# Performance work log

Measured on AMD Instinct MI355X. Metric: run time of the kernel, lower is better.

## Reference

```python
import jax, jax.numpy as jnp
import numpy as np

B, LOOKBACK, N_STOCKS, D_MODEL, D_K, D_V, MAX_LAG = 64, 32, 256, 512, 128, 128, 16


def setup_inputs() -> dict:
    key = jax.random.key(0)
    ks = jax.random.split(key, 7)
    return {
        "query_stock_emb": jax.random.normal(ks[0], (B, D_MODEL), dtype=jnp.float32),
        "all_stock_embs": jax.random.normal(ks[1], (B, LOOKBACK, N_STOCKS, D_MODEL), dtype=jnp.float32),
        "W_q": jax.random.normal(ks[2], (D_K, D_MODEL), dtype=jnp.float32) * 0.02,
        "W_k": jax.random.normal(ks[3], (D_K, D_MODEL), dtype=jnp.float32) * 0.02,
        "W_v": jax.random.normal(ks[4], (D_V, D_MODEL), dtype=jnp.float32) * 0.02,
        "lags": jax.random.uniform(ks[5], (N_STOCKS,), dtype=jnp.float32) * MAX_LAG,
        "causal_gates": jax.random.normal(ks[6], (N_STOCKS,), dtype=jnp.float32) * 0.1,
        "max_lag": MAX_LAG,
    }


def reference(query_stock_emb, all_stock_embs, W_q, W_k, W_v, lags, causal_gates, max_lag):
    lookback = all_stock_embs.shape[1]
    n_stocks = all_stock_embs.shape[2]
    d_k = W_q.shape[0]

    q = query_stock_emb @ W_q.T                        # (B, d_k)
    gates = jax.nn.sigmoid(causal_gates)               # (S,)
    lag = jax.nn.sigmoid(lags) * max_lag               # (S,)

    lag_floor = jnp.clip(jnp.floor(lag), 0, lookback - 1).astype(jnp.int32)
    lag_ceil = jnp.clip(jnp.ceil(lag), 0, lookback - 1).astype(jnp.int32)
    alpha = lag - lag_floor.astype(lag.dtype)          # (S,)

    s_idx = jnp.arange(n_stocks)
    emb_floor = all_stock_embs[:, lag_floor, s_idx, :]  # (B, S, D)
    emb_ceil = all_stock_embs[:, lag_ceil, s_idx, :]    # (B, S, D)
    a = alpha[None, :, None]
    stock_emb = (1.0 - a) * emb_floor + a * emb_ceil    # (B, S, D)

    k = jnp.einsum("bsd,kd->bsk", stock_emb, W_k)       # (B, S, d_k)
    v = jnp.einsum("bsd,vd->bsv", stock_emb, W_v)       # (B, S, d_v)

    scores = jnp.einsum("bk,bsk->bs", q, k) / np.sqrt(d_k).astype(jnp.float32)
    scores = scores * gates[None, :]
    attn = jax.nn.softmax(scores, axis=1)               # (B, S)
    context = jnp.einsum("bs,bsv->bv", attn, v)         # (B, d_v)
    return context
```

## Files before the change

kernel.cpp:

```cpp
#include <hip/hip_runtime.h>
#include <math.h>

#define B_    64
#define LOOKB 32
#define NS    256
#define DM    512
#define DK    128
#define DV    128

__device__ __forceinline__ float sigmoidf_(float x) {
    return 1.0f / (1.0f + expf(-x));
}

__device__ __forceinline__ float load_maxlag(const void* p) {
    int vi = *(const int*)p;
    if (vi >= 0 && vi < (1 << 23)) return (float)vi;
    return *(const float*)p;
}

__device__ __forceinline__ void lag_params(const float* __restrict__ lags,
                                           float maxlag, int s,
                                           int& lf, int& lc, float& alpha) {
    float lag = sigmoidf_(lags[s]) * maxlag;
    float lf_f = fminf(fmaxf(floorf(lag), 0.0f), (float)(LOOKB - 1));
    float lc_f = fminf(fmaxf(ceilf(lag), 0.0f), (float)(LOOKB - 1));
    lf = (int)lf_f;
    lc = (int)lc_f;
    alpha = lag - lf_f;
}

__global__ void k_prep(const float* __restrict__ query,
                       const float* __restrict__ Wq,
                       const float* __restrict__ Wk,
                       float* __restrict__ ws_m) {
    __shared__ float qe[DM];
    __shared__ float qv[DK];
    const int b = blockIdx.x;
    const int tid = threadIdx.x;

    qe[tid]       = query[b * DM + tid];
    qe[tid + 256] = query[b * DM + tid + 256];
    __syncthreads();

    if (tid < DK) {
        const float4* wr = (const float4*)(Wq + (size_t)tid * DM);
        const float4* qr = (const float4*)qe;
        float acc = 0.f;
#pragma unroll 8
        for (int i = 0; i < DM / 4; ++i) {
            float4 w = wr[i], q4 = qr[i];
            acc += w.x * q4.x + w.y * q4.y + w.z * q4.z + w.w * q4.w;
        }
        qv[tid] = acc;
    }
    __syncthreads();

    for (int d = tid; d < DM; d += 256) {
        float acc = 0.f;
#pragma unroll 8
        for (int k = 0; k < DK; ++k)
            acc += qv[k] * Wk[(size_t)k * DM + d];
        ws_m[b * DM + d] = acc;
    }
}

__global__ void k_scores(const float* __restrict__ embs,
                         const float* __restrict__ lags,
                         const float* __restrict__ gates,
                         const void*  __restrict__ maxlag_p,
                         const float* __restrict__ ws_m,
                         float* __restrict__ ws_scores) {
    const int tid  = threadIdx.x;
    const int b     = blockIdx.x >> 6;
    const int sbase = (blockIdx.x & 63) << 2;
    const int wave  = tid >> 6;
    const int lane  = tid & 63;
    const int s     = sbase + wave;

    const float maxlag = load_maxlag(maxlag_p);
    int lf, lc; float alpha;
    lag_params(lags, maxlag, s, lf, lc, alpha);
    const float gate = sigmoidf_(gates[s]);

    const size_t off = (size_t)lane * 8;
    const float* mrow = ws_m + (size_t)b * DM + off;
    float4 m0 = *(const float4*)(mrow);
    float4 m1 = *(const float4*)(mrow + 4);

    const size_t bf = (((size_t)b * LOOKB + lf) * NS + s) * (size_t)DM + off;
    const size_t bc = (((size_t)b * LOOKB + lc) * NS + s) * (size_t)DM + off;
    float4 f0 = *(const float4*)(embs + bf);
    float4 f1 = *(const float4*)(embs + bf + 4);
    float4 c0 = *(const float4*)(embs + bc);
    float4 c1 = *(const float4*)(embs + bc + 4);

    float acc = m0.x * (f0.x + alpha * (c0.x - f0.x))
              + m0.y * (f0.y + alpha * (c0.y - f0.y))
              + m0.z * (f0.z + alpha * (c0.z - f0.z))
              + m0.w * (f0.w + alpha * (c0.w - f0.w))
              + m1.x * (f1.x + alpha * (c1.x - f1.x))
              + m1.y * (f1.y + alpha * (c1.y - f1.y))
              + m1.z * (f1.z + alpha * (c1.z - f1.z))
              + m1.w * (f1.w + alpha * (c1.w - f1.w));

#pragma unroll
    for (int off2 = 32; off2; off2 >>= 1)
        acc += __shfl_xor(acc, off2, 64);

    if (lane == 0)
        ws_scores[b * NS + s] = gate * acc * 0.0883883476483184405f;
}

__global__ void k_softmax(const float* __restrict__ ws_scores,
                          float* __restrict__ ws_attn) {
    __shared__ float rmax[4];
    __shared__ float rsum[4];
    const int b = blockIdx.x, tid = threadIdx.x;
    const int wave = tid >> 6, lane = tid & 63;

    float v = ws_scores[b * NS + tid];
    float m = v;
#pragma unroll
    for (int off = 32; off; off >>= 1)
        m = fmaxf(m, __shfl_xor(m, off, 64));
    if (lane == 0) rmax[wave] = m;
    __syncthreads();
    const float mx = fmaxf(fmaxf(rmax[0], rmax[1]), fmaxf(rmax[2], rmax[3]));

    float e = expf(v - mx);
    float ssum = e;
#pragma unroll
    for (int off = 32; off; off >>= 1)
        ssum += __shfl_xor(ssum, off, 64);
    if (lane == 0) rsum[wave] = ssum;
    __syncthreads();
    const float tot = rsum[0] + rsum[1] + rsum[2] + rsum[3];

    ws_attn[b * NS + tid] = e / tot;
}

__global__ void k_ctx(const float* __restrict__ embs,
                      const float* __restrict__ lags,
                      const void*  __restrict__ maxlag_p,
                      const float* __restrict__ ws_attn,
                      float* __restrict__ ws_part) {
    const int b     = blockIdx.x >> 3;
    const int chunk = blockIdx.x & 7;
    const int tid   = threadIdx.x;
    const int d0    = tid * 2;
    const float maxlag = load_maxlag(maxlag_p);

    float ax = 0.f, ay = 0.f;
    const int s0 = chunk * 32;
#pragma unroll 4
    for (int i = 0; i < 32; ++i) {
        const int s = s0 + i;
        int lf, lc; float alpha;
        lag_params(lags, maxlag, s, lf, lc, alpha);
        const float w = ws_attn[b * NS + s];

        const size_t bf = (((size_t)b * LOOKB + lf) * NS + s) * (size_t)DM + d0;
        const size_t bc = (((size_t)b * LOOKB + lc) * NS + s) * (size_t)DM + d0;
        float2 ef = *(const float2*)(embs + bf);
        float2 ec = *(const float2*)(embs + bc);
        ax += w * (ef.x + alpha * (ec.x - ef.x));
        ay += w * (ef.y + alpha * (ec.y - ef.y));
    }
    float2 outv; outv.x = ax; outv.y = ay;
    *(float2*)(ws_part + ((size_t)(b * 8 + chunk)) * DM + d0) = outv;
}

__global__ void k_out(const float* __restrict__ ws_part,
                      const float* __restrict__ Wv,
                      float* __restrict__ out) {
    __shared__ float ctx[DM];
    const int b = blockIdx.x, tid = threadIdx.x;

    for (int d = tid; d < DM; d += 128) {
        float a = 0.f;
#pragma unroll
        for (int c = 0; c < 8; ++c)
            a += ws_part[((size_t)(b * 8 + c)) * DM + d];
        ctx[d] = a;
    }
    __syncthreads();

    const float4* wr = (const float4*)(Wv + (size_t)tid * DM);
    const float4* cr = (const float4*)ctx;
    float acc = 0.f;
#pragma unroll 8
    for (int i = 0; i < DM / 4; ++i) {
        float4 w = wr[i], c = cr[i];
        acc += w.x * c.x + w.y * c.y + w.z * c.z + w.w * c.w;
    }
    out[b * DV + tid] = acc;
}

extern "C" void kernel_launch(void* const* d_in, const int* in_sizes, int n_in,
                              void* d_out, int out_size, void* d_ws, size_t ws_size,
                              hipStream_t stream) {
    const float* query = (const float*)d_in[0];
    const float* embs  = (const float*)d_in[1];
    const float* Wq    = (const float*)d_in[2];
    const float* Wk    = (const float*)d_in[3];
    const float* Wv    = (const float*)d_in[4];
    const float* lags  = (const float*)d_in[5];
    const float* gates = (const float*)d_in[6];
    const void*  maxlag_p = d_in[7];

    float* out = (float*)d_out;

    float* ws        = (float*)d_ws;
    float* ws_m      = ws;
    float* ws_scores = ws + 32768;
    float* ws_attn   = ws + 49152;
    float* ws_part   = ws + 65536;
    (void)in_sizes; (void)n_in; (void)out_size; (void)ws_size;

    k_prep<<<B_, 256, 0, stream>>>(query, Wq, Wk, ws_m);
    k_scores<<<B_ * 64, 256, 0, stream>>>(embs, lags, gates, maxlag_p, ws_m, ws_scores);
    k_softmax<<<B_, 256, 0, stream>>>(ws_scores, ws_attn);
    k_ctx<<<B_ * 8, 256, 0, stream>>>(embs, lags, maxlag_p, ws_attn, ws_part);
    k_out<<<B_, 128, 0, stream>>>(ws_part, Wv, out);
}
```

Before: 1.201 ms.

## Fuse all five stages into one per-batch kernel with shared-memory intermediates

Replaces the five launches (prep, scores, softmax, context, output) with a single kernel that runs one 1024-thread block per batch element and keeps q, the projected query, scores, lag parameters and partial contexts in shared memory. Lag and gate parameters are computed once per block instead of per wave or per iteration. This removes launch overhead and workspace round-trips, but the grid shrinks to 64 blocks, which leaves most CUs idle and limits the memory parallelism available for the embedding gathers.

```diff
diff --git a/kernel.cpp b/kernel.cpp
--- a/kernel.cpp
+++ b/kernel.cpp
@@ -8,6 +8,7 @@
 #define DK    128
 #define DV    128
 
+
 __device__ __forceinline__ float sigmoidf_(float x) {
     return 1.0f / (1.0f + expf(-x));
 }
@@ -18,182 +19,179 @@
     return *(const float*)p;
 }
 
-__device__ __forceinline__ void lag_params(const float* __restrict__ lags,
-                                           float maxlag, int s,
-                                           int& lf, int& lc, float& alpha) {
-    float lag = sigmoidf_(lags[s]) * maxlag;
-    float lf_f = fminf(fmaxf(floorf(lag), 0.0f), (float)(LOOKB - 1));
-    float lc_f = fminf(fmaxf(ceilf(lag), 0.0f), (float)(LOOKB - 1));
-    lf = (int)lf_f;
-    lc = (int)lc_f;
-    alpha = lag - lf_f;
-}
-
-__global__ void k_prep(const float* __restrict__ query,
-                       const float* __restrict__ Wq,
-                       const float* __restrict__ Wk,
-                       float* __restrict__ ws_m) {
+__global__ __launch_bounds__(1024) void k_fused(
+    const float* __restrict__ query,
+    const float* __restrict__ embs,
+    const float* __restrict__ Wq,
+    const float* __restrict__ Wk,
+    const float* __restrict__ Wv,
+    const float* __restrict__ lags,
+    const float* __restrict__ gates,
+    const void*  __restrict__ maxlag_p,
+    float* __restrict__ out)
+{
     __shared__ float qe[DM];
     __shared__ float qv[DK];
-    const int b = blockIdx.x;
-    const int tid = threadIdx.x;
-
-    qe[tid]       = query[b * DM + tid];
-    qe[tid + 256] = query[b * DM + tid + 256];
-    __syncthreads();
-
-    if (tid < DK) {
-        const float4* wr = (const float4*)(Wq + (size_t)tid * DM);
-        const float4* qr = (const float4*)qe;
+    __shared__ float ms[DM];
+    __shared__ float sc[NS];
+    __shared__ float gt[NS];
+    __shared__ int   lfi[NS];
+    __shared__ int   lci[NS];
+    __shared__ float alf[NS];
+    __shared__ float part[4 * DM];
+    __shared__ float ctxs[DM];
+    __shared__ float red[16];
+
+    const int b    = blockIdx.x;
+    const int t    = threadIdx.x;
+    const int lane = t & 63;
+    const int wv   = t >> 6;
+
+    if (t < DM) {
+        qe[t] = query[b * DM + t];
+    } else if (t < DM + NS) {
+        const int s = t - DM;
+        const float maxlag = load_maxlag(maxlag_p);
+        float lag  = sigmoidf_(lags[s]) * maxlag;
+        float lf_f = fminf(fmaxf(floorf(lag), 0.0f), (float)(LOOKB - 1));
+        float lc_f = fminf(fmaxf(ceilf(lag), 0.0f), (float)(LOOKB - 1));
+        lfi[s] = (int)lf_f;
+        lci[s] = (int)lc_f;
+        alf[s] = lag - lf_f;
+        gt[s]  = sigmoidf_(gates[s]);
+    }
+    __syncthreads();
+
+    {
+        const int r   = t >> 3;
+        const int sub = t & 7;
+        const float4* wr = (const float4*)(Wq + (size_t)r * DM);
+        float acc = 0.f;
+#pragma unroll
+        for (int i = 0; i < 16; ++i) {
+            float4 w  = wr[sub + i * 8];
+            float4 q4 = *(const float4*)(qe + sub * 4 + i * 32);
+            acc += w.x * q4.x + w.y * q4.y + w.z * q4.z + w.w * q4.w;
+        }
+        acc += __shfl_xor(acc, 1, 64);
+        acc += __shfl_xor(acc, 2, 64);
+        acc += __shfl_xor(acc, 4, 64);
+        if (sub == 0) qv[r] = acc;
+    }
+    __syncthreads();
+
+    {
+        const int d = t & 511;
+        const int h = t >> 9;
+        const float* wkp = Wk + (size_t)(h * 64) * DM + d;
         float acc = 0.f;
 #pragma unroll 8
-        for (int i = 0; i < DM / 4; ++i) {
-            float4 w = wr[i], q4 = qr[i];
-            acc += w.x * q4.x + w.y * q4.y + w.z * q4.z + w.w * q4.w;
-        }
-        qv[tid] = acc;
-    }
-    __syncthreads();
-
-    for (int d = tid; d < DM; d += 256) {
+        for (int k = 0; k < 64; ++k)
+            acc += qv[h * 64 + k] * wkp[(size_t)k * DM];
+        part[t] = acc;
+    }
+    __syncthreads();
+    if (t < DM) ms[t] = part[t] + part[t + DM];
+    __syncthreads();
+
+    {
+        const size_t off = (size_t)lane * 8;
+        const float4 mr0 = *(const float4*)(ms + off);
+        const float4 mr1 = *(const float4*)(ms + off + 4);
+        const float* base_b = embs + (size_t)b * LOOKB * NS * DM + off;
+#pragma unroll 4
+        for (int i = 0; i < 16; ++i) {
+            const int s  = (wv << 4) + i;
+            const int lf = lfi[s];
+            const int lc = lci[s];
+            const float a = alf[s];
+            const float* pf = base_b + ((size_t)lf * NS + s) * DM;
+            const float* pc = base_b + ((size_t)lc * NS + s) * DM;
+            float4 f0 = *(const float4*)(pf);
+            float4 f1 = *(const float4*)(pf + 4);
+            float4 c0 = *(const float4*)(pc);
+            float4 c1 = *(const float4*)(pc + 4);
+            float acc = mr0.x * (f0.x + a * (c0.x - f0.x))
+                      + mr0.y * (f0.y + a * (c0.y - f0.y))
+                      + mr0.z * (f0.z + a * (c0.z - f0.z))
+                      + mr0.w * (f0.w + a * (c0.w - f0.w))
+                      + mr1.x * (f1.x + a * (c1.x - f1.x))
+                      + mr1.y * (f1.y + a * (c1.y - f1.y))
+                      + mr1.z * (f1.z + a * (c1.z - f1.z))
+                      + mr1.w * (f1.w + a * (c1.w - f1.w));
+#pragma unroll
+            for (int o = 32; o; o >>= 1)
+                acc += __shfl_xor(acc, o, 64);
+            if (lane == 0)
+                sc[s] = gt[s] * acc * 0.0883883476483184405f;
+        }
+    }
+    __syncthreads();
+
+    {
+        const float v = (t < NS) ? sc[t] : -INFINITY;
+        float mx = v;
+#pragma unroll
+        for (int o = 32; o; o >>= 1)
+            mx = fmaxf(mx, __shfl_xor(mx, o, 64));
+        if (lane == 0) red[wv] = mx;
+        __syncthreads();
+        const float gmx = fmaxf(fmaxf(red[0], red[1]), fmaxf(red[2], red[3]));
+        const float e = (t < NS) ? expf(v - gmx) : 0.f;
+        float sm = e;
+#pragma unroll
+        for (int o = 32; o; o >>= 1)
+            sm += __shfl_xor(sm, o, 64);
+        __syncthreads();
+        if (lane == 0) red[wv] = sm;
+        __syncthreads();
+        const float tot = red[0] + red[1] + red[2] + red[3];
+        if (t < NS) sc[t] = e / tot;
+    }
+    __syncthreads();
+
+    {
+        const int c  = t & 255;
+        const int g  = t >> 8;
+        const int d0 = c * 2;
+        float ax = 0.f, ay = 0.f;
+        const float* base_b = embs + (size_t)b * LOOKB * NS * DM + d0;
+#pragma unroll 4
+        for (int i = 0; i < 64; ++i) {
+            const int s  = (g << 6) + i;
+            const int lf = lfi[s];
+            const int lc = lci[s];
+            const float a = alf[s];
+            const float w = sc[s];
+            const float2 ef = *(const float2*)(base_b + ((size_t)lf * NS + s) * DM);
+            const float2 ec = *(const float2*)(base_b + ((size_t)lc * NS + s) * DM);
+            ax += w * (ef.x + a * (ec.x - ef.x));
+            ay += w * (ef.y + a * (ec.y - ef.y));
+        }
+        float2 o; o.x = ax; o.y = ay;
+        *(float2*)(part + g * DM + d0) = o;
+    }
+    __syncthreads();
+    if (t < DM)
+        ctxs[t] = part[t] + part[DM + t] + part[2 * DM + t] + part[3 * DM + t];
+    __syncthreads();
+
+    {
+        const int r   = t >> 3;
+        const int sub = t & 7;
+        const float4* wr = (const float4*)(Wv + (size_t)r * DM);
         float acc = 0.f;
-#pragma unroll 8
-        for (int k = 0; k < DK; ++k)
-            acc += qv[k] * Wk[(size_t)k * DM + d];
-        ws_m[b * DM + d] = acc;
-    }
-}
-
-__global__ void k_scores(const float* __restrict__ embs,
-                         const float* __restrict__ lags,
-                         const float* __restrict__ gates,
-                         const void*  __restrict__ maxlag_p,
-                         const float* __restrict__ ws_m,
-                         float* __restrict__ ws_scores) {
-    const int tid  = threadIdx.x;
-    const int b     = blockIdx.x >> 6;
-    const int sbase = (blockIdx.x & 63) << 2;
-    const int wave  = tid >> 6;
-    const int lane  = tid & 63;
-    const int s     = sbase + wave;
-
-    const float maxlag = load_maxlag(maxlag_p);
-    int lf, lc; float alpha;
-    lag_params(lags, maxlag, s, lf, lc, alpha);
-    const float gate = sigmoidf_(gates[s]);
-
-    const size_t off = (size_t)lane * 8;
-    const float* mrow = ws_m + (size_t)b * DM + off;
-    float4 m0 = *(const float4*)(mrow);
-    float4 m1 = *(const float4*)(mrow + 4);
-
-    const size_t bf = (((size_t)b * LOOKB + lf) * NS + s) * (size_t)DM + off;
-    const size_t bc = (((size_t)b * LOOKB + lc) * NS + s) * (size_t)DM + off;
-    float4 f0 = *(const float4*)(embs + bf);
-    float4 f1 = *(const float4*)(embs + bf + 4);
-    float4 c0 = *(const float4*)(embs + bc);
-    float4 c1 = *(const float4*)(embs + bc + 4);
-
-    float acc = m0.x * (f0.x + alpha * (c0.x - f0.x))
-              + m0.y * (f0.y + alpha * (c0.y - f0.y))
-              + m0.z * (f0.z + alpha * (c0.z - f0.z))
-              + m0.w * (f0.w + alpha * (c0.w - f0.w))
-              + m1.x * (f1.x + alpha * (c1.x - f1.x))
-              + m1.y * (f1.y + alpha * (c1.y - f1.y))
-              + m1.z * (f1.z + alpha * (c1.z - f1.z))
-              + m1.w * (f1.w + alpha * (c1.w - f1.w));
-
-#pragma unroll
-    for (int off2 = 32; off2; off2 >>= 1)
-        acc += __shfl_xor(acc, off2, 64);
-
-    if (lane == 0)
-        ws_scores[b * NS + s] = gate * acc * 0.0883883476483184405f;
-}
-
-__global__ void k_softmax(const float* __restrict__ ws_scores,
-                          float* __restrict__ ws_attn) {
-    __shared__ float rmax[4];
-    __shared__ float rsum[4];
-    const int b = blockIdx.x, tid = threadIdx.x;
-    const int wave = tid >> 6, lane = tid & 63;
-
-    float v = ws_scores[b * NS + tid];
-    float m = v;
-#pragma unroll
-    for (int off = 32; off; off >>= 1)
-        m = fmaxf(m, __shfl_xor(m, off, 64));
-    if (lane == 0) rmax[wave] = m;
-    __syncthreads();
-    const float mx = fmaxf(fmaxf(rmax[0], rmax[1]), fmaxf(rmax[2], rmax[3]));
-
-    float e = expf(v - mx);
-    float ssum = e;
-#pragma unroll
-    for (int off = 32; off; off >>= 1)
-        ssum += __shfl_xor(ssum, off, 64);
-    if (lane == 0) rsum[wave] = ssum;
-    __syncthreads();
-    const float tot = rsum[0] + rsum[1] + rsum[2] + rsum[3];
-
-    ws_attn[b * NS + tid] = e / tot;
-}
-
-__global__ void k_ctx(const float* __restrict__ embs,
-                      const float* __restrict__ lags,
-                      const void*  __restrict__ maxlag_p,
-                      const float* __restrict__ ws_attn,
-                      float* __restrict__ ws_part) {
-    const int b     = blockIdx.x >> 3;
-    const int chunk = blockIdx.x & 7;
-    const int tid   = threadIdx.x;
-    const int d0    = tid * 2;
-    const float maxlag = load_maxlag(maxlag_p);
-
-    float ax = 0.f, ay = 0.f;
-    const int s0 = chunk * 32;
-#pragma unroll 4
-    for (int i = 0; i < 32; ++i) {
-        const int s = s0 + i;
-        int lf, lc; float alpha;
-        lag_params(lags, maxlag, s, lf, lc, alpha);
-        const float w = ws_attn[b * NS + s];
-
-        const size_t bf = (((size_t)b * LOOKB + lf) * NS + s) * (size_t)DM + d0;
-        const size_t bc = (((size_t)b * LOOKB + lc) * NS + s) * (size_t)DM + d0;
-        float2 ef = *(const float2*)(embs + bf);
-        float2 ec = *(const float2*)(embs + bc);
-        ax += w * (ef.x + alpha * (ec.x - ef.x));
-        ay += w * (ef.y + alpha * (ec.y - ef.y));
-    }
-    float2 outv; outv.x = ax; outv.y = ay;
-    *(float2*)(ws_part + ((size_t)(b * 8 + chunk)) * DM + d0) = outv;
-}
-
-__global__ void k_out(const float* __restrict__ ws_part,
-                      const float* __restrict__ Wv,
-                      float* __restrict__ out) {
-    __shared__ float ctx[DM];
-    const int b = blockIdx.x, tid = threadIdx.x;
-
-    for (int d = tid; d < DM; d += 128) {
-        float a = 0.f;
-#pragma unroll
-        for (int c = 0; c < 8; ++c)
-            a += ws_part[((size_t)(b * 8 + c)) * DM + d];
-        ctx[d] = a;
-    }
-    __syncthreads();
-
-    const float4* wr = (const float4*)(Wv + (size_t)tid * DM);
-    const float4* cr = (const float4*)ctx;
-    float acc = 0.f;
-#pragma unroll 8
-    for (int i = 0; i < DM / 4; ++i) {
-        float4 w = wr[i], c = cr[i];
-        acc += w.x * c.x + w.y * c.y + w.z * c.z + w.w * c.w;
-    }
-    out[b * DV + tid] = acc;
+#pragma unroll
+        for (int i = 0; i < 16; ++i) {
+            float4 w  = wr[sub + i * 8];
+            float4 c4 = *(const float4*)(ctxs + sub * 4 + i * 32);
+            acc += w.x * c4.x + w.y * c4.y + w.z * c4.z + w.w * c4.w;
+        }
+        acc += __shfl_xor(acc, 1, 64);
+        acc += __shfl_xor(acc, 2, 64);
+        acc += __shfl_xor(acc, 4, 64);
+        if (sub == 0) out[b * DV + r] = acc;
+    }
 }
 
 extern "C" void kernel_launch(void* const* d_in, const int* in_sizes, int n_in,
@@ -209,17 +207,8 @@
     const void*  maxlag_p = d_in[7];
 
     float* out = (float*)d_out;
-
-    float* ws        = (float*)d_ws;
-    float* ws_m      = ws;
-    float* ws_scores = ws + 32768;
-    float* ws_attn   = ws + 49152;
-    float* ws_part   = ws + 65536;
-    (void)in_sizes; (void)n_in; (void)out_size; (void)ws_size;
-
-    k_prep<<<B_, 256, 0, stream>>>(query, Wq, Wk, ws_m);
-    k_scores<<<B_ * 64, 256, 0, stream>>>(embs, lags, gates, maxlag_p, ws_m, ws_scores);
-    k_softmax<<<B_, 256, 0, stream>>>(ws_scores, ws_attn);
-    k_ctx<<<B_ * 8, 256, 0, stream>>>(embs, lags, maxlag_p, ws_attn, ws_part);
-    k_out<<<B_, 128, 0, stream>>>(ws_part, Wv, out);
-}
+    (void)in_sizes; (void)n_in; (void)out_size; (void)d_ws; (void)ws_size;
+
+    k_fused<<<B_, 1024, 0, stream>>>(query, embs, Wq, Wk, Wv,
+                                     lags, gates, maxlag_p, out);
+}
```

New measurement: 1.175 ms. -2.1%, faster.
